# Performance work log

Measured on AMD Instinct MI355X. Metric: run time of the kernel, lower is better.

The kernel has to match this reference:

```python
import jax, jax.numpy as jnp
import numpy as np
from jax import lax


def setup_inputs() -> dict:
    key = jax.random.key(0)
    ks = jax.random.split(key, 11)
    B, S, V, E, H = 32, 256, 32000, 128, 128
    return {
        "sequence": jax.random.randint(ks[0], (B, S), 0, V),
        "encoder_output": jax.random.normal(ks[1], (B, S, H), jnp.float32),
        "encoder_output_hidden": jax.random.normal(ks[2], (1, B, H), jnp.float32),
        "encoder_output_cell": jax.random.normal(ks[3], (1, B, H), jnp.float32),
        "emb": jax.random.normal(ks[4], (V, E), jnp.float32) * 0.02,
        "W_ih": jax.random.normal(ks[5], (4 * H, E + H), jnp.float32) * 0.05,
        "b_ih": jax.random.normal(ks[6], (4 * H,), jnp.float32) * 0.05,
        "W_hh": jax.random.normal(ks[7], (4 * H, H), jnp.float32) * 0.05,
        "b_hh": jax.random.normal(ks[8], (4 * H,), jnp.float32) * 0.05,
        "W_pred": jax.random.normal(ks[9], (V, H), jnp.float32) * 0.05,
        "b_pred": jax.random.normal(ks[10], (V,), jnp.float32) * 0.05,
    }


def reference(sequence, encoder_output, encoder_output_hidden, encoder_output_cell,
              emb, W_ih, b_ih, W_hh, b_hh, W_pred, b_pred):
    B, S = sequence.shape
    H = W_hh.shape[1]
    x = emb[sequence]                      # [B, S, E]
    h0 = encoder_output_hidden[0]          # [B, H] fixed state fed every step
    c0 = encoder_output_cell[0]            # [B, H]
    # gate contribution from the fixed hidden state is constant over time
    hh = h0 @ W_hh.T + b_hh                # [B, 4H]

    def step(h_prev, x_t):
        inp = jnp.concatenate([x_t, h_prev], axis=1)   # [B, E+H]
        gates = inp @ W_ih.T + b_ih + hh               # [B, 4H]
        i, f, g, o = jnp.split(gates, 4, axis=1)       # torch LSTMCell order
        c = jax.nn.sigmoid(f) * c0 + jax.nn.sigmoid(i) * jnp.tanh(g)
        h = jax.nn.sigmoid(o) * jnp.tanh(c)
        return h, h

    h_init = jnp.zeros((B, H), x.dtype)
    _, hs = lax.scan(step, h_init, jnp.swapaxes(x, 0, 1))  # hs: [S, B, H]
    hs = jnp.swapaxes(hs, 0, 1)                            # [B, S, H]
    logits = hs @ W_pred.T + b_pred                        # [B, S, V]
    return jax.nn.log_softmax(logits, axis=-1)
```

## Files before the change

### kernel.cpp

```cpp
#include <hip/hip_runtime.h>

typedef short bf16x8 __attribute__((ext_vector_type(8)));
typedef float f32x4  __attribute__((ext_vector_type(4)));
typedef unsigned short u16;
typedef unsigned short u16x8 __attribute__((ext_vector_type(8)));

#define NB   32
#define NS   256
#define NV   32000
#define NE   128
#define NH   128
#define NR   8192
#define NG   512
#define NCHUNK 500

__device__ __forceinline__ float sigm(float x){
    return __builtin_amdgcn_rcpf(1.0f + __expf(-x));
}
__device__ __forceinline__ float tanh_fast(float x){
    return 1.0f - 2.0f*__builtin_amdgcn_rcpf(1.0f + __expf(2.0f*x));
}

__device__ __forceinline__ u16 f2bf(float x){
    unsigned u = __float_as_uint(x);
    unsigned r = (u + 0x7FFFu + ((u >> 16) & 1u)) >> 16;
    return (u16)r;
}

__device__ __forceinline__ void lds_barrier(){
    asm volatile("s_waitcnt lgkmcnt(0)" ::: "memory");
    __builtin_amdgcn_s_barrier();
    __builtin_amdgcn_sched_barrier(0);
}


__global__ __launch_bounds__(256) void khh(const float* __restrict__ h0,
                                           const float* __restrict__ W_hh,
                                           const float* __restrict__ b_ih,
                                           const float* __restrict__ b_hh,
                                           float* __restrict__ hh){
    int idx = blockIdx.x*256 + threadIdx.x;
    int b = idx >> 9, j = idx & 511;
    const float4* h4 = (const float4*)(h0 + b*NH);
    const float4* w4 = (const float4*)(W_hh + j*NH);
    float acc = b_ih[j] + b_hh[j];
    #pragma unroll
    for (int k = 0; k < 32; ++k){
        float4 a = h4[k], w = w4[k];
        acc += a.x*w.x + a.y*w.y + a.z*w.z + a.w*w.w;
    }
    hh[idx] = acc;
}

__global__ __launch_bounds__(256) void kwb(const float* __restrict__ src, u16* __restrict__ dst){
    int a8 = blockIdx.x*256 + threadIdx.x;
    int a = a8 * 8;
    int rb = a >> 13; int blk = (a >> 9) & 15; int lane = (a >> 3) & 63;
    int q = blk & 3, kk = blk >> 2;
    int l15 = lane & 15, l4 = lane >> 4;
    int m = rb*64 + q*16 + l15;
    int j = kk*32 + l4*8;
    const float* s = src + (size_t)m*NH + j;
    float4 x = *(const float4*)s, y = *(const float4*)(s + 4);
    u16x8 o;
    o[0]=f2bf(x.x); o[1]=f2bf(x.y); o[2]=f2bf(x.z); o[3]=f2bf(x.w);
    o[4]=f2bf(y.x); o[5]=f2bf(y.y); o[6]=f2bf(y.z); o[7]=f2bf(y.w);
    *(u16x8*)&dst[a] = o;
}

__global__ __launch_bounds__(256) void ktr(const u16* __restrict__ src, u16* __restrict__ dst){
    int a8 = blockIdx.x*256 + threadIdx.x;
    int a = a8 * 8;
    int rb = a >> 13; int blk = (a >> 9) & 15; int lane = (a >> 3) & 63;
    int q = blk & 3, kk = blk >> 2;
    int l15 = lane & 15, l4 = lane >> 4;
    int m = rb*64 + q*16 + l15;
    int j = kk*32 + l4*8;
    *(uint4*)&dst[a] = *(const uint4*)&src[(size_t)m*NH + j];
}

__global__ __launch_bounds__(256) void kxg(const int* __restrict__ seq,
                                           const float* __restrict__ emb,
                                           const float* __restrict__ W_ih,
                                           float* __restrict__ xg){
    __shared__ float4 xs[16][32];
    int m0 = blockIdx.x * 16;
    int t = threadIdx.x;
    int r = t >> 4, k4 = t & 15;
    int tok = seq[m0 + r];
    xs[r][k4]      = *(const float4*)(emb + (size_t)tok*NE + k4*4);
    xs[r][k4 + 16] = *(const float4*)(emb + (size_t)tok*NE + (k4+16)*4);
    __syncthreads();
    int j0 = t, j1 = t + 256;
    const float4* w0 = (const float4*)(W_ih + (size_t)j0*256);
    const float4* w1 = (const float4*)(W_ih + (size_t)j1*256);
    float acc0[16], acc1[16];
    #pragma unroll
    for (int r2 = 0; r2 < 16; ++r2){ acc0[r2]=0.f; acc1[r2]=0.f; }
    #pragma unroll
    for (int k = 0; k < 32; ++k){
        float4 wa = w0[k], wb = w1[k];
        #pragma unroll
        for (int r2 = 0; r2 < 16; ++r2){
            float4 xv = xs[r2][k];
            acc0[r2] += xv.x*wa.x + xv.y*wa.y + xv.z*wa.z + xv.w*wa.w;
            acc1[r2] += xv.x*wb.x + xv.y*wb.y + xv.z*wb.z + xv.w*wb.w;
        }
    }
    #pragma unroll
    for (int r2 = 0; r2 < 16; ++r2){
        xg[(size_t)(m0+r2)*NG + j0] = acc0[r2];
        xg[(size_t)(m0+r2)*NG + j1] = acc1[r2];
    }
}

#define LSTM_STEP(S, XA, XB) {                                                  \
    float a0=0.f,a1=0.f,a2=0.f,a3=0.f,b0=0.f,b1=0.f,b2=0.f,b3=0.f;              \
    const uint4* h4 = (const uint4*)&hsh2[(S) & 1][0];                          \
    _Pragma("unroll")                                                           \
    for (int k = 0; k < 16; ++k){                                               \
        uint4 hv = h4[k];                                                       \
        asm("v_dot2_f32_bf16 %0, %1, %2, %0" : "+v"(a0) : "v"(hv.x), "v"(w2a[4*k+0])); \
        asm("v_dot2_f32_bf16 %0, %1, %2, %0" : "+v"(a1) : "v"(hv.y), "v"(w2a[4*k+1])); \
        asm("v_dot2_f32_bf16 %0, %1, %2, %0" : "+v"(a2) : "v"(hv.z), "v"(w2a[4*k+2])); \
        asm("v_dot2_f32_bf16 %0, %1, %2, %0" : "+v"(a3) : "v"(hv.w), "v"(w2a[4*k+3])); \
        asm("v_dot2_f32_bf16 %0, %1, %2, %0" : "+v"(b0) : "v"(hv.x), "v"(w2b[4*k+0])); \
        asm("v_dot2_f32_bf16 %0, %1, %2, %0" : "+v"(b1) : "v"(hv.y), "v"(w2b[4*k+1])); \
        asm("v_dot2_f32_bf16 %0, %1, %2, %0" : "+v"(b2) : "v"(hv.z), "v"(w2b[4*k+2])); \
        asm("v_dot2_f32_bf16 %0, %1, %2, %0" : "+v"(b3) : "v"(hv.w), "v"(w2b[4*k+3])); \
    }                                                                           \
    float gateA = hba + (XA) + ((a0+a1)+(a2+a3));                               \
    float gateB = hbb + (XB) + ((b0+b1)+(b2+b3));                               \
    float fg = __shfl_xor(gateA, 1);                                            \
    float og = __shfl_xor(gateB, 1);                                            \
    float cc = sigm(fg)*c0r + sigm(gateA)*tanh_fast(gateB);                     \
    float h  = sigm(og)*tanh_fast(cc);                                          \
    u16 hb16 = f2bf(h);                                                         \
    if (!odd) hrow[(S)*NH + r] = hb16;                                          \
    unsigned hpart = __shfl_xor((unsigned)hb16, 2);                             \
    if ((t & 3) == 0) hsh2[((S) & 1) ^ 1][r >> 1] = (hpart << 16) | (unsigned)hb16; \
    lds_barrier();                                                              \
}

__global__ __launch_bounds__(256, 1) void klstm(const float* __restrict__ xg,
                                                const float* __restrict__ hh,
                                                const float* __restrict__ W_ih,
                                                const float* __restrict__ c0,
                                                u16* __restrict__ hs){
    __shared__ __align__(16) unsigned hsh2[2][64];
    int b = blockIdx.x, t = threadIdx.x;
    int r = t >> 1, odd = t & 1;
    int gA = r + (odd ? 128 : 0);
    int gB = gA + 256;
    unsigned w2a[64], w2b[64];
    const float2* wra = (const float2*)(W_ih + (size_t)gA*256 + 128);
    const float2* wrb = (const float2*)(W_ih + (size_t)gB*256 + 128);
    #pragma unroll
    for (int k = 0; k < 64; ++k){
        float2 va = wra[k], vb = wrb[k];
        w2a[k] = ((unsigned)f2bf(va.y) << 16) | (unsigned)f2bf(va.x);
        w2b[k] = ((unsigned)f2bf(vb.y) << 16) | (unsigned)f2bf(vb.x);
    }
    float hba = hh[b*NG + gA];
    float hbb = hh[b*NG + gB];
    float c0r = c0[b*NH + r];
    if (t < 64){ hsh2[0][t] = 0u; }
    __syncthreads();
    const float* xrow = xg + (size_t)b*NS*NG;
    u16* hrow = hs + (size_t)b*NS*NH;
    float x0a = xrow[gA],        x0b = xrow[gB];
    float x1a = xrow[NG+gA],     x1b = xrow[NG+gB];
    float x2a = xrow[2*NG+gA],   x2b = xrow[2*NG+gB];
    float x3a = xrow[3*NG+gA],   x3b = xrow[3*NG+gB];
    for (int s4 = 0; s4 < NS; s4 += 4){
        float n0a=0.f,n0b=0.f,n1a=0.f,n1b=0.f,n2a=0.f,n2b=0.f,n3a=0.f,n3b=0.f;
        if (s4 + 4 < NS){
            const float* xn = xrow + (size_t)(s4+4)*NG;
            n0a = xn[gA];      n0b = xn[gB];
            n1a = xn[NG+gA];   n1b = xn[NG+gB];
            n2a = xn[2*NG+gA]; n2b = xn[2*NG+gB];
            n3a = xn[3*NG+gA]; n3b = xn[3*NG+gB];
        }
        LSTM_STEP(s4+0, x0a, x0b);
        LSTM_STEP(s4+1, x1a, x1b);
        LSTM_STEP(s4+2, x2a, x2b);
        LSTM_STEP(s4+3, x3a, x3b);
        x0a=n0a; x0b=n0b; x1a=n1a; x1b=n1b;
        x2a=n2a; x2b=n2b; x3a=n3a; x3b=n3b;
    }
}


#define LOAD_A(DST, R) {                                                        \
    int rbA = (mbase >> 6) + (R)*2 + wr;                                        \
    const u16* pa = hsbF + (size_t)rbA*8192 + lane*8;                           \
    _Pragma("unroll")                                                           \
    for (int q = 0; q < 4; ++q)                                                 \
        _Pragma("unroll")                                                       \
        for (int kk = 0; kk < 4; ++kk)                                          \
            DST[q][kk] = *(const bf16x8*)&pa[(kk*4 + q)*512];                   \
}

template<int PASS>
__global__ __launch_bounds__(256, 2) void kgemm(const u16* __restrict__ hsbF,
                                                const u16* __restrict__ wbF,
                                                const float* __restrict__ bpred,
                                                const float* __restrict__ lse,
                                                float* __restrict__ psum,
                                                float* __restrict__ out){
    int tid = threadIdx.x;
    int bid = blockIdx.x;
    int c    = bid >> 1;
    int half = bid & 1;
    int n0 = c * 128;
    int mbase = half * 4096;

    int wid = tid >> 6, lane = tid & 63;
    int wr = wid >> 1, wc = wid & 1;
    int l15 = lane & 15, l4 = lane >> 4;
    const float L2E = 1.44269504f;
    float4 bp4[4];
    #pragma unroll
    for (int f = 0; f < 4; ++f){
        bp4[f] = *(const float4*)&bpred[n0 + wc*64 + f*16 + l4*4];
        if (PASS == 0){
            bp4[f].x *= L2E; bp4[f].y *= L2E; bp4[f].z *= L2E; bp4[f].w *= L2E;
        }
    }

    bf16x8 bfr[4][4];
    {
        int rbB = c*2 + wc;
        const u16* pb = wbF + (size_t)rbB*8192 + lane*8;
        #pragma unroll
        for (int f = 0; f < 4; ++f)
            #pragma unroll
            for (int kk = 0; kk < 4; ++kk)
                bfr[f][kk] = *(const bf16x8*)&pb[(kk*4 + f)*512];
    }

    bf16x8 af[4][4];
    LOAD_A(af, 0);
    for (int r = 0; r < 32; ++r){
        f32x4 acc[4][4];
        #pragma unroll
        for (int q = 0; q < 4; ++q)
            #pragma unroll
            for (int f = 0; f < 4; ++f)
                acc[q][f] = (f32x4){0.f,0.f,0.f,0.f};
        #pragma unroll
        for (int f = 0; f < 4; ++f)
            #pragma unroll
            for (int q = 0; q < 4; ++q)
                #pragma unroll
                for (int kk = 0; kk < 4; ++kk)
                    acc[q][f] = __builtin_amdgcn_mfma_f32_16x16x32_bf16(
                        bfr[f][kk], af[q][kk], acc[q][f], 0, 0, 0);

        if (r + 1 < 32) LOAD_A(af, r+1);

        if (PASS == 0){
            float lsum[4];
            #pragma unroll
            for (int q = 0; q < 4; ++q){
                float s = 0.f;
                #pragma unroll
                for (int f = 0; f < 4; ++f)
                    #pragma unroll
                    for (int rr = 0; rr < 4; ++rr){
                        float tt = fmaf(acc[q][f][rr], L2E, bp4[f][rr]);
                        float e; asm("v_exp_f32 %0, %1" : "=v"(e) : "v"(tt));
                        s += e;
                    }
                s += __shfl_xor(s, 16);
                s += __shfl_xor(s, 32);
                lsum[q] = s;
            }
            float sv = (l4 == 0) ? lsum[0] : (l4 == 1) ? lsum[1]
                     : (l4 == 2) ? lsum[2] : lsum[3];
            psum[(size_t)(c*2 + wc)*NR + mbase + r*128 + wr*64 + lane] = sv;
        } else {
            #pragma unroll
            for (int q = 0; q < 4; ++q){
                int grow = mbase + r*128 + wr*64 + q*16 + l15;
                float lw = lse[grow];
                float* orow = out + (size_t)grow*NV + n0 + wc*64 + l4*4;
                #pragma unroll
                for (int f = 0; f < 4; ++f){
                    f32x4 v;
                    v[0] = acc[q][f][0] + bp4[f].x - lw;
                    v[1] = acc[q][f][1] + bp4[f].y - lw;
                    v[2] = acc[q][f][2] + bp4[f].z - lw;
                    v[3] = acc[q][f][3] + bp4[f].w - lw;
                    *(f32x4*)&orow[f*16] = v;
                }
            }
        }
    }
}

__global__ __launch_bounds__(256) void klse(const float* __restrict__ psum,
                                            float* __restrict__ lse){
    __shared__ float red[32][8];
    int t = threadIdx.x;
    int row = blockIdx.x*32 + (t >> 3);
    int grp = t & 7;
    float S = 0.f;
    for (int cc = grp; cc < NCHUNK; cc += 8)
        S += psum[(size_t)cc*NR + row];
    red[t >> 3][grp] = S;
    __syncthreads();
    if (grp == 0){
        float s2 = 0.f;
        #pragma unroll
        for (int g = 0; g < 8; ++g) s2 += red[t >> 3][g];
        lse[row] = __logf(s2);
    }
}

extern "C" void kernel_launch(void* const* d_in, const int* in_sizes, int n_in,
                              void* d_out, int out_size, void* d_ws, size_t ws_size,
                              hipStream_t stream){
    (void)in_sizes; (void)n_in; (void)out_size; (void)ws_size;
    const int*   seq    = (const int*)d_in[0];
    const float* h0     = (const float*)d_in[2];
    const float* c0     = (const float*)d_in[3];
    const float* emb    = (const float*)d_in[4];
    const float* W_ih   = (const float*)d_in[5];
    const float* b_ih   = (const float*)d_in[6];
    const float* W_hh   = (const float*)d_in[7];
    const float* b_hh   = (const float*)d_in[8];
    const float* W_pred = (const float*)d_in[9];
    const float* b_pred = (const float*)d_in[10];
    float* out = (float*)d_out;

    char* ws = (char*)d_ws;
    float* xg   = (float*)(ws);
    float* psum = (float*)(ws);
    float* hh   = (float*)(ws + 16777216);
    u16*   hsb  = (u16*)  (ws + 16842752);
    u16*   wbbF = (u16*)  (ws + 18939904);
    float* lse  = (float*)(ws + 27131904);
    u16*   hsbF = (u16*)  (ws + 27164672);

    khh<<<64, 256, 0, stream>>>(h0, W_hh, b_ih, b_hh, hh);
    kwb<<<2000, 256, 0, stream>>>(W_pred, wbbF);
    kxg<<<512, 256, 0, stream>>>(seq, emb, W_ih, xg);
    klstm<<<32, 256, 0, stream>>>(xg, hh, W_ih, c0, hsb);
    ktr<<<1024, 256, 0, stream>>>(hsb, hsbF);
    kgemm<0><<<500, 256, 0, stream>>>(hsbF, wbbF, b_pred, nullptr, psum, out);
    klse<<<256, 256, 0, stream>>>(psum, lse);
    kgemm<1><<<500, 256, 0, stream>>>(hsbF, wbbF, b_pred, lse, psum, out);
}
```

Before: 549.7 us.

## Split LSTM recurrence K-dimension across 4 lanes with 512-thread blocks

Restructures the serial LSTM kernel so each hidden unit is handled by 4 lanes, each computing a quarter of the K reduction for all four gates, followed by xor-shuffle reductions. Block size doubles to 512 threads, halving the per-thread dot-product chain length on each recurrent step. Each lane now loads only 16 bytes of h per gate group, and the hidden-state output is written as packed pairs. The cost is extra shuffles and more waves per step barrier.

After: 554.6 us. About the same (+0.9%).

```diff
diff --git a/kernel.cpp b/kernel.cpp
--- a/kernel.cpp
+++ b/kernel.cpp
@@ -114,79 +114,89 @@
     }
 }
 
-#define LSTM_STEP(S, XA, XB) {                                                  \
-    float a0=0.f,a1=0.f,a2=0.f,a3=0.f,b0=0.f,b1=0.f,b2=0.f,b3=0.f;              \
+#define DOT16(ACC, B) {                                                         \
+    asm("v_dot2_f32_bf16 %0, %1, %2, %0" : "+v"(ACC) : "v"(hq0.x), "v"(w2[(B)+0])); \
+    asm("v_dot2_f32_bf16 %0, %1, %2, %0" : "+v"(ACC) : "v"(hq0.y), "v"(w2[(B)+1])); \
+    asm("v_dot2_f32_bf16 %0, %1, %2, %0" : "+v"(ACC) : "v"(hq0.z), "v"(w2[(B)+2])); \
+    asm("v_dot2_f32_bf16 %0, %1, %2, %0" : "+v"(ACC) : "v"(hq0.w), "v"(w2[(B)+3])); \
+    asm("v_dot2_f32_bf16 %0, %1, %2, %0" : "+v"(ACC) : "v"(hq1.x), "v"(w2[(B)+4])); \
+    asm("v_dot2_f32_bf16 %0, %1, %2, %0" : "+v"(ACC) : "v"(hq1.y), "v"(w2[(B)+5])); \
+    asm("v_dot2_f32_bf16 %0, %1, %2, %0" : "+v"(ACC) : "v"(hq1.z), "v"(w2[(B)+6])); \
+    asm("v_dot2_f32_bf16 %0, %1, %2, %0" : "+v"(ACC) : "v"(hq1.w), "v"(w2[(B)+7])); \
+    asm("v_dot2_f32_bf16 %0, %1, %2, %0" : "+v"(ACC) : "v"(hq2.x), "v"(w2[(B)+8])); \
+    asm("v_dot2_f32_bf16 %0, %1, %2, %0" : "+v"(ACC) : "v"(hq2.y), "v"(w2[(B)+9])); \
+    asm("v_dot2_f32_bf16 %0, %1, %2, %0" : "+v"(ACC) : "v"(hq2.z), "v"(w2[(B)+10])); \
+    asm("v_dot2_f32_bf16 %0, %1, %2, %0" : "+v"(ACC) : "v"(hq2.w), "v"(w2[(B)+11])); \
+    asm("v_dot2_f32_bf16 %0, %1, %2, %0" : "+v"(ACC) : "v"(hq3.x), "v"(w2[(B)+12])); \
+    asm("v_dot2_f32_bf16 %0, %1, %2, %0" : "+v"(ACC) : "v"(hq3.y), "v"(w2[(B)+13])); \
+    asm("v_dot2_f32_bf16 %0, %1, %2, %0" : "+v"(ACC) : "v"(hq3.z), "v"(w2[(B)+14])); \
+    asm("v_dot2_f32_bf16 %0, %1, %2, %0" : "+v"(ACC) : "v"(hq3.w), "v"(w2[(B)+15])); \
+}
+
+#define LSTM_STEP(S, XV) {                                                      \
     const uint4* h4 = (const uint4*)&hsh2[(S) & 1][0];                          \
-    _Pragma("unroll")                                                           \
-    for (int k = 0; k < 16; ++k){                                               \
-        uint4 hv = h4[k];                                                       \
-        asm("v_dot2_f32_bf16 %0, %1, %2, %0" : "+v"(a0) : "v"(hv.x), "v"(w2a[4*k+0])); \
-        asm("v_dot2_f32_bf16 %0, %1, %2, %0" : "+v"(a1) : "v"(hv.y), "v"(w2a[4*k+1])); \
-        asm("v_dot2_f32_bf16 %0, %1, %2, %0" : "+v"(a2) : "v"(hv.z), "v"(w2a[4*k+2])); \
-        asm("v_dot2_f32_bf16 %0, %1, %2, %0" : "+v"(a3) : "v"(hv.w), "v"(w2a[4*k+3])); \
-        asm("v_dot2_f32_bf16 %0, %1, %2, %0" : "+v"(b0) : "v"(hv.x), "v"(w2b[4*k+0])); \
-        asm("v_dot2_f32_bf16 %0, %1, %2, %0" : "+v"(b1) : "v"(hv.y), "v"(w2b[4*k+1])); \
-        asm("v_dot2_f32_bf16 %0, %1, %2, %0" : "+v"(b2) : "v"(hv.z), "v"(w2b[4*k+2])); \
-        asm("v_dot2_f32_bf16 %0, %1, %2, %0" : "+v"(b3) : "v"(hv.w), "v"(w2b[4*k+3])); \
+    uint4 hq0 = h4[p4+0], hq1 = h4[p4+1], hq2 = h4[p4+2], hq3 = h4[p4+3];       \
+    float s0=0.f, s1=0.f, s2=0.f, s3=0.f;                                       \
+    DOT16(s0, 0); DOT16(s1, 16); DOT16(s2, 32); DOT16(s3, 48);                  \
+    float hbx = hba + (XV);                                                     \
+    s0 += (p == 0) ? hbx : 0.f;                                                 \
+    s1 += (p == 1) ? hbx : 0.f;                                                 \
+    s2 += (p == 2) ? hbx : 0.f;                                                 \
+    s3 += (p == 3) ? hbx : 0.f;                                                 \
+    s0 += __shfl_xor(s0, 1); s0 += __shfl_xor(s0, 2);                           \
+    s1 += __shfl_xor(s1, 1); s1 += __shfl_xor(s1, 2);                           \
+    s2 += __shfl_xor(s2, 1); s2 += __shfl_xor(s2, 2);                           \
+    s3 += __shfl_xor(s3, 1); s3 += __shfl_xor(s3, 2);                           \
+    float cc = sigm(s1)*c0r + sigm(s0)*tanh_fast(s2);                           \
+    float h  = sigm(s3)*tanh_fast(cc);                                          \
+    u16 hb16 = f2bf(h);                                                         \
+    unsigned hp = __shfl_xor((unsigned)hb16, 4);              \
+    if ((t & 7) == 0){                                                          \
+        unsigned pair = (hp << 16) | (unsigned)hb16;                            \
+        hsh2[((S) & 1) ^ 1][r >> 1] = pair;                                     \
+        *(unsigned*)&hrow[(S)*NH + r] = pair;                                   \
     }                                                                           \
-    float gateA = hba + (XA) + ((a0+a1)+(a2+a3));                               \
-    float gateB = hbb + (XB) + ((b0+b1)+(b2+b3));                               \
-    float fg = __shfl_xor(gateA, 1);                                            \
-    float og = __shfl_xor(gateB, 1);                                            \
-    float cc = sigm(fg)*c0r + sigm(gateA)*tanh_fast(gateB);                     \
-    float h  = sigm(og)*tanh_fast(cc);                                          \
-    u16 hb16 = f2bf(h);                                                         \
-    if (!odd) hrow[(S)*NH + r] = hb16;                                          \
-    unsigned hpart = __shfl_xor((unsigned)hb16, 2);                             \
-    if ((t & 3) == 0) hsh2[((S) & 1) ^ 1][r >> 1] = (hpart << 16) | (unsigned)hb16; \
     lds_barrier();                                                              \
 }
 
-__global__ __launch_bounds__(256, 1) void klstm(const float* __restrict__ xg,
+__global__ __launch_bounds__(512, 1) void klstm(const float* __restrict__ xg,
                                                 const float* __restrict__ hh,
                                                 const float* __restrict__ W_ih,
                                                 const float* __restrict__ c0,
                                                 u16* __restrict__ hs){
     __shared__ __align__(16) unsigned hsh2[2][64];
     int b = blockIdx.x, t = threadIdx.x;
-    int r = t >> 1, odd = t & 1;
-    int gA = r + (odd ? 128 : 0);
-    int gB = gA + 256;
-    unsigned w2a[64], w2b[64];
-    const float2* wra = (const float2*)(W_ih + (size_t)gA*256 + 128);
-    const float2* wrb = (const float2*)(W_ih + (size_t)gB*256 + 128);
-    #pragma unroll
-    for (int k = 0; k < 64; ++k){
-        float2 va = wra[k], vb = wrb[k];
-        w2a[k] = ((unsigned)f2bf(va.y) << 16) | (unsigned)f2bf(va.x);
-        w2b[k] = ((unsigned)f2bf(vb.y) << 16) | (unsigned)f2bf(vb.x);
-    }
-    float hba = hh[b*NG + gA];
-    float hbb = hh[b*NG + gB];
+    int r = t >> 2;
+    int p = t & 3;
+    int p4 = p * 4;
+    unsigned w2[64];
+    #pragma unroll
+    for (int j = 0; j < 4; ++j){
+        const float2* wrj = (const float2*)(W_ih + (size_t)(j*NH + r)*256 + 128 + p*32);
+        #pragma unroll
+        for (int k = 0; k < 16; ++k){
+            float2 v = wrj[k];
+            w2[j*16 + k] = ((unsigned)f2bf(v.y) << 16) | (unsigned)f2bf(v.x);
+        }
+    }
+    float hba = hh[b*NG + p*NH + r];
     float c0r = c0[b*NH + r];
     if (t < 64){ hsh2[0][t] = 0u; }
     __syncthreads();
-    const float* xrow = xg + (size_t)b*NS*NG;
+    const float* xrow = xg + (size_t)b*NS*NG + p*NH + r;
     u16* hrow = hs + (size_t)b*NS*NH;
-    float x0a = xrow[gA],        x0b = xrow[gB];
-    float x1a = xrow[NG+gA],     x1b = xrow[NG+gB];
-    float x2a = xrow[2*NG+gA],   x2b = xrow[2*NG+gB];
-    float x3a = xrow[3*NG+gA],   x3b = xrow[3*NG+gB];
+    float xv0 = xrow[0], xv1 = xrow[NG], xv2 = xrow[2*NG], xv3 = xrow[3*NG];
     for (int s4 = 0; s4 < NS; s4 += 4){
-        float n0a=0.f,n0b=0.f,n1a=0.f,n1b=0.f,n2a=0.f,n2b=0.f,n3a=0.f,n3b=0.f;
+        float n0=0.f, n1=0.f, n2=0.f, n3=0.f;
         if (s4 + 4 < NS){
             const float* xn = xrow + (size_t)(s4+4)*NG;
-            n0a = xn[gA];      n0b = xn[gB];
-            n1a = xn[NG+gA];   n1b = xn[NG+gB];
-            n2a = xn[2*NG+gA]; n2b = xn[2*NG+gB];
-            n3a = xn[3*NG+gA]; n3b = xn[3*NG+gB];
-        }
-        LSTM_STEP(s4+0, x0a, x0b);
-        LSTM_STEP(s4+1, x1a, x1b);
-        LSTM_STEP(s4+2, x2a, x2b);
-        LSTM_STEP(s4+3, x3a, x3b);
-        x0a=n0a; x0b=n0b; x1a=n1a; x1b=n1b;
-        x2a=n2a; x2b=n2b; x3a=n3a; x3b=n3b;
+            n0 = xn[0]; n1 = xn[NG]; n2 = xn[2*NG]; n3 = xn[3*NG];
+        }
+        LSTM_STEP(s4+0, xv0);
+        LSTM_STEP(s4+1, xv1);
+        LSTM_STEP(s4+2, xv2);
+        LSTM_STEP(s4+3, xv3);
+        xv0=n0; xv1=n1; xv2=n2; xv3=n3;
     }
 }
 
@@ -346,7 +356,7 @@
     khh<<<64, 256, 0, stream>>>(h0, W_hh, b_ih, b_hh, hh);
     kwb<<<2000, 256, 0, stream>>>(W_pred, wbbF);
     kxg<<<512, 256, 0, stream>>>(seq, emb, W_ih, xg);
-    klstm<<<32, 256, 0, stream>>>(xg, hh, W_ih, c0, hsb);
+    klstm<<<32, 512, 0, stream>>>(xg, hh, W_ih, c0, hsb);
     ktr<<<1024, 256, 0, stream>>>(hsb, hsbF);
     kgemm<0><<<500, 256, 0, stream>>>(hsbF, wbbF, b_pred, nullptr, psum, out);
     klse<<<256, 256, 0, stream>>>(psum, lse);
```
